# Kernel tuning notes

Measured on AMD Instinct MI355X. Metric: run time of the kernel, lower is better.

Reference implementation:

```python
import jax, jax.numpy as jnp
import numpy as np

N_EMB = 512
DIM = 64
BETA = 0.25
EPS = 1e-10


def setup_inputs() -> dict:
    key = jax.random.key(0)
    k1, k2 = jax.random.split(key)
    z = jax.random.normal(k1, (32, 64, 64, 64), dtype=jnp.float32)  # (B, C=DIM, H, W)
    # embedding weight initialized uniform(-1/K, 1/K) as in the module
    weight = jax.random.uniform(k2, (N_EMB, DIM), dtype=jnp.float32,
                                minval=-1.0 / N_EMB, maxval=1.0 / N_EMB)
    return {"z": z, "weight": weight}


def reference(z, weight):
    # (B,C,H,W) -> (B,H,W,C)
    zp = jnp.transpose(z, (0, 2, 3, 1))
    zf = zp.reshape(-1, DIM)  # (N, D)
    # pairwise squared distances ||z||^2 + ||e||^2 - 2 z.e  -> (N, K)
    d = (jnp.sum(zf * zf, axis=1, keepdims=True)
         + jnp.sum(weight * weight, axis=1)
         - 2.0 * zf @ weight.T)
    codebook = jnp.argmin(d, axis=1)  # (N,)
    encodings = jax.nn.one_hot(codebook, N_EMB, dtype=zf.dtype)  # (N, K)
    # direct gather == one_hot @ weight (same math, efficient form)
    z_q = weight[codebook].reshape(zp.shape)
    sg = jax.lax.stop_gradient
    loss = jnp.mean((sg(z_q) - zp) ** 2) + BETA * jnp.mean((z_q - sg(zp)) ** 2)
    # straight-through estimator
    z_q = zp + sg(z_q - zp)
    e_mean = jnp.mean(encodings, axis=0)
    perplexity = jnp.exp(-jnp.sum(e_mean * jnp.log(e_mean + EPS)))
    z_q = jnp.transpose(z_q, (0, 3, 1, 2))  # back to (B,C,H,W)
    return (loss, z_q, perplexity, encodings, codebook)
```

## Files before the change

### kernel.cpp

```cpp
#include <hip/hip_runtime.h>
#include <math.h>

#define NK 512
#define DIMV 64
#define NPTS (32*64*64)
#define NELEM (32*64*64*64)
#define WT_STRIDE 132

#define OFF_LOSS 0
#define OFF_ZQ   1
#define OFF_PERP (1 + NELEM)
#define OFF_ENC  (2 + NELEM)
#define OFF_CB   (2 + NELEM + (size_t)NPTS * NK)

__global__ __launch_bounds__(256) void vq_main(const float* __restrict__ zg,
                                               const float* __restrict__ wg,
                                               float* __restrict__ out,
                                               int* __restrict__ hist,
                                               double* __restrict__ lossAcc) {
    const int t = threadIdx.x;
    const int blk = blockIdx.x;
    const int b = blk >> 6;
    const int h = blk & 63;

    __shared__ __align__(16) float zt[64 * 64];
    __shared__ __align__(16) float wt[64 * WT_STRIDE];
    __shared__ float aRow[64];
    __shared__ float bnd[128];
    __shared__ int   idxs[64];
    __shared__ float rsum[256];

    float* zqt  = wt;
    float* redv = wt + 4096;
    int*   redi = (int*)(wt + 4096 + 16 * 66);

    {
        const int w = t & 63;
        const int c0 = t >> 6;
        const size_t base = (size_t)b * 262144 + (size_t)h * 64;
        #pragma unroll
        for (int c = c0; c < 64; c += 4)
            zt[c * 64 + w] = zg[base + (size_t)c * 4096 + w];
    }
    __syncthreads();

    if (t < 64) {
        float s = 0.f;
        for (int d = 0; d < 64; ++d) {
            float v = zt[d * 64 + t];
            s = __fadd_rn(s, __fmul_rn(v, v));
        }
        aRow[t] = s;
    }
    __syncthreads();

    const int tx = t & 15;
    const int ty = t >> 4;
    const int ty4 = ty * 4;
    const int tx8 = tx * 8;

    float av[4];
    #pragma unroll
    for (int i = 0; i < 4; ++i) av[i] = aRow[ty4 + i];

    float best[4];
    int bidx[4];
    #pragma unroll
    for (int i = 0; i < 4; ++i) { best[i] = INFINITY; bidx[i] = 0; }

    for (int chunk = 0; chunk < 4; ++chunk) {
        {
            const int d = t & 63, kk0 = t >> 6;
            #pragma unroll
            for (int kk = kk0; kk < 128; kk += 4)
                wt[d * WT_STRIDE + kk] = wg[((size_t)(chunk * 128 + kk)) * 64 + d];
        }
        __syncthreads();

        if (t < 128) {
            float s = 0.f;
            for (int d = 0; d < 64; ++d) {
                float v = wt[d * WT_STRIDE + t];
                s = __fadd_rn(s, __fmul_rn(v, v));
            }
            bnd[t] = s;
        }
        __syncthreads();

        float acc[4][8];
        #pragma unroll
        for (int i = 0; i < 4; ++i)
            #pragma unroll
            for (int j = 0; j < 8; ++j) acc[i][j] = 0.f;

        const float* ztp = zt + ty4;
        const float* wtp = wt + tx8;
        #pragma unroll 4
        for (int d = 0; d < 64; ++d) {
            const float4 zv = *(const float4*)(ztp + d * 64);
            const float4 w0 = *(const float4*)(wtp + d * WT_STRIDE);
            const float4 w1 = *(const float4*)(wtp + d * WT_STRIDE + 4);
            const float zr[4] = {zv.x, zv.y, zv.z, zv.w};
            const float wr[8] = {w0.x, w0.y, w0.z, w0.w, w1.x, w1.y, w1.z, w1.w};
            #pragma unroll
            for (int i = 0; i < 4; ++i)
                #pragma unroll
                for (int j = 0; j < 8; ++j)
                    acc[i][j] = fmaf(zr[i], wr[j], acc[i][j]);
        }

        #pragma unroll
        for (int i = 0; i < 4; ++i) {
            #pragma unroll
            for (int j = 0; j < 8; ++j) {
                float dist = __fsub_rn(__fadd_rn(av[i], bnd[tx8 + j]), 2.0f * acc[i][j]);
                int k = chunk * 128 + tx8 + j;
                if (dist < best[i]) { best[i] = dist; bidx[i] = k; }
            }
        }
        __syncthreads();
    }

    #pragma unroll
    for (int i = 0; i < 4; ++i) {
        redv[tx * 66 + ty4 + i] = best[i];
        redi[tx * 64 + ty4 + i] = bidx[i];
    }
    __syncthreads();

    if (t < 64) {
        float bv = redv[t];
        int bi = redi[t];
        #pragma unroll
        for (int x = 1; x < 16; ++x) {
            float v = redv[x * 66 + t];
            int ii = redi[x * 64 + t];
            if (v < bv || (v == bv && ii < bi)) { bv = v; bi = ii; }
        }
        idxs[t] = bi;
        atomicAdd(&hist[bi], 1);
        out[OFF_CB + (size_t)blk * 64 + t] = (float)bi;
        const float4* wr4 = (const float4*)(wg + (size_t)bi * 64);
        #pragma unroll
        for (int q = 0; q < 16; ++q) {
            float4 v = wr4[q];
            zqt[(4 * q + 0) * 64 + t] = v.x;
            zqt[(4 * q + 1) * 64 + t] = v.y;
            zqt[(4 * q + 2) * 64 + t] = v.z;
            zqt[(4 * q + 3) * 64 + t] = v.w;
        }
    }
    __syncthreads();

    {
        float4* enc = (float4*)(out + OFF_ENC + (size_t)blk * 64 * NK);
        for (int e = t; e < 64 * 128; e += 256) {
            int r = e >> 7, c4 = e & 127;
            int idx = idxs[r];
            float4 v = make_float4(0.f, 0.f, 0.f, 0.f);
            if ((idx >> 2) == c4) ((float*)&v)[idx & 3] = 1.0f;
            enc[(size_t)r * 128 + c4] = v;
        }
    }

    float lsum = 0.f;
    {
        float* zq = out + OFF_ZQ + (size_t)b * 262144 + (size_t)h * 64;
        for (int e = t; e < 4096; e += 256) {
            int p = e & 63, d = e >> 6;
            float zv = zt[d * 64 + p];
            float qv = zqt[d * 64 + p];
            float diff = __fsub_rn(qv, zv);
            lsum = __fadd_rn(lsum, __fmul_rn(diff, diff));
            zq[(size_t)d * 4096 + p] = __fadd_rn(zv, diff);
        }
    }
    rsum[t] = lsum;
    __syncthreads();
    for (int s = 128; s > 0; s >>= 1) {
        if (t < s) rsum[t] += rsum[t + s];
        __syncthreads();
    }
    if (t == 0) atomicAdd(lossAcc, (double)rsum[0]);
}

__global__ __launch_bounds__(512) void vq_finalize(const int* __restrict__ hist,
                                                   const double* __restrict__ lossAcc,
                                                   float* __restrict__ out) {
    __shared__ float sh[512];
    const int t = threadIdx.x;
    float p = (float)hist[t] / (float)NPTS;
    sh[t] = __fmul_rn(p, logf(__fadd_rn(p, 1e-10f)));
    __syncthreads();
    for (int s = 256; s > 0; s >>= 1) {
        if (t < s) sh[t] += sh[t + s];
        __syncthreads();
    }
    if (t == 0) {
        float m = (float)(*lossAcc / (double)NELEM);
        out[OFF_LOSS] = __fadd_rn(m, __fmul_rn(0.25f, m));
        out[OFF_PERP] = expf(-sh[0]);
    }
}

extern "C" void kernel_launch(void* const* d_in, const int* in_sizes, int n_in,
                              void* d_out, int out_size, void* d_ws, size_t ws_size,
                              hipStream_t stream) {
    const float* z = (const float*)d_in[0];
    const float* w = (const float*)d_in[1];
    float* out = (float*)d_out;
    int* hist = (int*)d_ws;
    double* lossAcc = (double*)((char*)d_ws + 2048);

    hipMemsetAsync(d_ws, 0, 4096, stream);
    vq_main<<<2048, 256, 0, stream>>>(z, w, out, hist, lossAcc);
    vq_finalize<<<1, 512, 0, stream>>>(hist, lossAcc, out);
}
```

Before: 472.1 us.

## Precompute transposed codebook and norms, prefetch chunks, vectorize and nontemporal stores

A new prep kernel transposes the codebook into a d-major buffer and computes the codebook norms once, so each main block no longer does strided transposing loads or recomputes norms for every chunk. The main loop prefetches the next codebook chunk into registers while computing the current one, which removes a barrier per chunk. The thread-to-tile mapping is swapped. The encodings and z_q outputs are written with nontemporal vectorized stores, and the loss reduction uses wavefront shuffles instead of a shared-memory tree. The costs are one extra small kernel launch, more registers for the prefetch, and a 128-float LDS stride without padding that may cause bank conflicts.

```diff
diff --git a/kernel.cpp b/kernel.cpp
--- a/kernel.cpp
+++ b/kernel.cpp
@@ -2,10 +2,10 @@
 #include <math.h>
 
 #define NK 512
-#define DIMV 64
 #define NPTS (32*64*64)
 #define NELEM (32*64*64*64)
-#define WT_STRIDE 132
+
+typedef float nvf4 __attribute__((ext_vector_type(4)));
 
 #define OFF_LOSS 0
 #define OFF_ZQ   1
@@ -13,8 +13,41 @@
 #define OFF_ENC  (2 + NELEM)
 #define OFF_CB   (2 + NELEM + (size_t)NPTS * NK)
 
+
+__global__ __launch_bounds__(256) void vq_prep(const float* __restrict__ wg,
+                                               float* __restrict__ wT,
+                                               float* __restrict__ bnd) {
+    __shared__ float tl[64 * 65];
+    const int t = threadIdx.x;
+    const int kbase = blockIdx.x * 64;
+    #pragma unroll
+    for (int it = 0; it < 16; ++it) {
+        int i = it * 256 + t;
+        int k = i >> 6, d = i & 63;
+        tl[k * 65 + d] = wg[(size_t)(kbase + k) * 64 + d];
+    }
+    __syncthreads();
+    #pragma unroll
+    for (int it = 0; it < 16; ++it) {
+        int j = it * 256 + t;
+        int d = j >> 6, kk = j & 63;
+        wT[(size_t)d * 512 + kbase + kk] = tl[kk * 65 + d];
+    }
+    if (t < 64) {
+        float s = 0.f;
+        #pragma unroll 4
+        for (int d = 0; d < 64; ++d) {
+            float v = tl[t * 65 + d];
+            s = __fadd_rn(s, __fmul_rn(v, v));
+        }
+        bnd[kbase + t] = s;
+    }
+}
+
 __global__ __launch_bounds__(256) void vq_main(const float* __restrict__ zg,
                                                const float* __restrict__ wg,
+                                               const float* __restrict__ wT,
+                                               const float* __restrict__ bndg,
                                                float* __restrict__ out,
                                                int* __restrict__ hist,
                                                double* __restrict__ lossAcc) {
@@ -24,15 +57,23 @@
     const int h = blk & 63;
 
     __shared__ __align__(16) float zt[64 * 64];
-    __shared__ __align__(16) float wt[64 * WT_STRIDE];
+    __shared__ __align__(16) float wt[64 * 128];
     __shared__ float aRow[64];
-    __shared__ float bnd[128];
     __shared__ int   idxs[64];
-    __shared__ float rsum[256];
+    __shared__ float wsum[4];
 
     float* zqt  = wt;
     float* redv = wt + 4096;
-    int*   redi = (int*)(wt + 4096 + 16 * 66);
+    int*   redi = (int*)(wt + 4096 + 16 * 68);
+
+    const float4* wT4 = (const float4*)wT;
+    float4* wt4 = (float4*)wt;
+    const int d0 = t >> 5, c4 = t & 31;
+
+    float4 pf[8];
+    #pragma unroll
+    for (int s = 0; s < 8; ++s)
+        pf[s] = wT4[(size_t)(d0 + s * 8) * 128 + c4];
 
     {
         const int w = t & 63;
@@ -56,50 +97,53 @@
 
     const int tx = t & 15;
     const int ty = t >> 4;
-    const int ty4 = ty * 4;
-    const int tx8 = tx * 8;
+    const int p0 = tx * 4;
+    const int ty8 = ty * 8;
 
     float av[4];
     #pragma unroll
-    for (int i = 0; i < 4; ++i) av[i] = aRow[ty4 + i];
+    for (int i = 0; i < 4; ++i) av[i] = aRow[p0 + i];
 
     float best[4];
     int bidx[4];
     #pragma unroll
     for (int i = 0; i < 4; ++i) { best[i] = INFINITY; bidx[i] = 0; }
 
-    for (int chunk = 0; chunk < 4; ++chunk) {
+    for (int c = 0; c < 4; ++c) {
+        if (c) __syncthreads();
+
+        #pragma unroll
+        for (int s = 0; s < 8; ++s)
+            wt4[(d0 + s * 8) * 32 + c4] = pf[s];
+
+        if (c < 3) {
+            #pragma unroll
+            for (int s = 0; s < 8; ++s)
+                pf[s] = wT4[(size_t)(d0 + s * 8) * 128 + (c + 1) * 32 + c4];
+        }
+
+        float bn[8];
         {
-            const int d = t & 63, kk0 = t >> 6;
-            #pragma unroll
-            for (int kk = kk0; kk < 128; kk += 4)
-                wt[d * WT_STRIDE + kk] = wg[((size_t)(chunk * 128 + kk)) * 64 + d];
+            const float4* bp = (const float4*)(bndg + c * 128 + ty8);
+            float4 b0 = bp[0], b1 = bp[1];
+            bn[0] = b0.x; bn[1] = b0.y; bn[2] = b0.z; bn[3] = b0.w;
+            bn[4] = b1.x; bn[5] = b1.y; bn[6] = b1.z; bn[7] = b1.w;
         }
         __syncthreads();
 
-        if (t < 128) {
-            float s = 0.f;
-            for (int d = 0; d < 64; ++d) {
-                float v = wt[d * WT_STRIDE + t];
-                s = __fadd_rn(s, __fmul_rn(v, v));
-            }
-            bnd[t] = s;
-        }
-        __syncthreads();
-
         float acc[4][8];
         #pragma unroll
         for (int i = 0; i < 4; ++i)
             #pragma unroll
             for (int j = 0; j < 8; ++j) acc[i][j] = 0.f;
 
-        const float* ztp = zt + ty4;
-        const float* wtp = wt + tx8;
+        const float* ztp = zt + p0;
+        const float* wtp = wt + ty8;
         #pragma unroll 4
         for (int d = 0; d < 64; ++d) {
             const float4 zv = *(const float4*)(ztp + d * 64);
-            const float4 w0 = *(const float4*)(wtp + d * WT_STRIDE);
-            const float4 w1 = *(const float4*)(wtp + d * WT_STRIDE + 4);
+            const float4 w0 = *(const float4*)(wtp + d * 128);
+            const float4 w1 = *(const float4*)(wtp + d * 128 + 4);
             const float zr[4] = {zv.x, zv.y, zv.z, zv.w};
             const float wr[8] = {w0.x, w0.y, w0.z, w0.w, w1.x, w1.y, w1.z, w1.w};
             #pragma unroll
@@ -113,18 +157,18 @@
         for (int i = 0; i < 4; ++i) {
             #pragma unroll
             for (int j = 0; j < 8; ++j) {
-                float dist = __fsub_rn(__fadd_rn(av[i], bnd[tx8 + j]), 2.0f * acc[i][j]);
-                int k = chunk * 128 + tx8 + j;
+                float dist = __fsub_rn(__fadd_rn(av[i], bn[j]), 2.0f * acc[i][j]);
+                int k = c * 128 + ty8 + j;
                 if (dist < best[i]) { best[i] = dist; bidx[i] = k; }
             }
         }
-        __syncthreads();
-    }
+    }
+    __syncthreads();
 
     #pragma unroll
     for (int i = 0; i < 4; ++i) {
-        redv[tx * 66 + ty4 + i] = best[i];
-        redi[tx * 64 + ty4 + i] = bidx[i];
+        redv[ty * 68 + p0 + i] = best[i];
+        redi[ty * 64 + p0 + i] = bidx[i];
     }
     __syncthreads();
 
@@ -133,7 +177,7 @@
         int bi = redi[t];
         #pragma unroll
         for (int x = 1; x < 16; ++x) {
-            float v = redv[x * 66 + t];
+            float v = redv[x * 68 + t];
             int ii = redi[x * 64 + t];
             if (v < bv || (v == bv && ii < bi)) { bv = v; bi = ii; }
         }
@@ -153,35 +197,44 @@
     __syncthreads();
 
     {
-        float4* enc = (float4*)(out + OFF_ENC + (size_t)blk * 64 * NK);
-        for (int e = t; e < 64 * 128; e += 256) {
-            int r = e >> 7, c4 = e & 127;
+        nvf4* enc = (nvf4*)(out + OFF_ENC + (size_t)blk * 64 * NK);
+        #pragma unroll
+        for (int it = 0; it < 32; ++it) {
+            int e = it * 256 + t;
+            int r = e >> 7, cc = e & 127;
             int idx = idxs[r];
-            float4 v = make_float4(0.f, 0.f, 0.f, 0.f);
-            if ((idx >> 2) == c4) ((float*)&v)[idx & 3] = 1.0f;
-            enc[(size_t)r * 128 + c4] = v;
+            nvf4 v = (nvf4)(0.f);
+            if ((idx >> 2) == cc) v[idx & 3] = 1.0f;
+            __builtin_nontemporal_store(v, &enc[(size_t)r * 128 + cc]);
         }
     }
 
     float lsum = 0.f;
     {
         float* zq = out + OFF_ZQ + (size_t)b * 262144 + (size_t)h * 64;
-        for (int e = t; e < 4096; e += 256) {
-            int p = e & 63, d = e >> 6;
-            float zv = zt[d * 64 + p];
-            float qv = zqt[d * 64 + p];
-            float diff = __fsub_rn(qv, zv);
-            lsum = __fadd_rn(lsum, __fmul_rn(diff, diff));
-            zq[(size_t)d * 4096 + p] = __fadd_rn(zv, diff);
-        }
-    }
-    rsum[t] = lsum;
-    __syncthreads();
-    for (int s = 128; s > 0; s >>= 1) {
-        if (t < s) rsum[t] += rsum[t + s];
-        __syncthreads();
-    }
-    if (t == 0) atomicAdd(lossAcc, (double)rsum[0]);
+        #pragma unroll
+        for (int it = 0; it < 4; ++it) {
+            int f = it * 256 + t;
+            int d = f >> 4, pp = (f & 15) * 4;
+            float4 zv = *(const float4*)(zt + d * 64 + pp);
+            float4 qv = *(const float4*)(zqt + d * 64 + pp);
+            nvf4 o;
+            float dx = __fsub_rn(qv.x, zv.x); lsum = __fadd_rn(lsum, __fmul_rn(dx, dx)); o[0] = __fadd_rn(zv.x, dx);
+            float dy = __fsub_rn(qv.y, zv.y); lsum = __fadd_rn(lsum, __fmul_rn(dy, dy)); o[1] = __fadd_rn(zv.y, dy);
+            float dz = __fsub_rn(qv.z, zv.z); lsum = __fadd_rn(lsum, __fmul_rn(dz, dz)); o[2] = __fadd_rn(zv.z, dz);
+            float dw = __fsub_rn(qv.w, zv.w); lsum = __fadd_rn(lsum, __fmul_rn(dw, dw)); o[3] = __fadd_rn(zv.w, dw);
+            __builtin_nontemporal_store(o, (nvf4*)(zq + (size_t)d * 4096 + pp));
+        }
+    }
+    #pragma unroll
+    for (int off = 32; off > 0; off >>= 1)
+        lsum += __shfl_down(lsum, off);
+    if ((t & 63) == 0) wsum[t >> 6] = lsum;
+    __syncthreads();
+    if (t == 0) {
+        float tot = (wsum[0] + wsum[1]) + (wsum[2] + wsum[3]);
+        atomicAdd(lossAcc, (double)tot);
+    }
 }
 
 __global__ __launch_bounds__(512) void vq_finalize(const int* __restrict__ hist,
@@ -211,8 +264,11 @@
     float* out = (float*)d_out;
     int* hist = (int*)d_ws;
     double* lossAcc = (double*)((char*)d_ws + 2048);
-
-    hipMemsetAsync(d_ws, 0, 4096, stream);
-    vq_main<<<2048, 256, 0, stream>>>(z, w, out, hist, lossAcc);
+    float* wT = (float*)((char*)d_ws + 4096);
+    float* bnd = wT + 64 * 512;
+
+    (void)hipMemsetAsync(d_ws, 0, 4096, stream);
+    vq_prep<<<8, 256, 0, stream>>>(w, wT, bnd);
+    vq_main<<<2048, 256, 0, stream>>>(z, w, wT, bnd, out, hist, lossAcc);
     vq_finalize<<<1, 512, 0, stream>>>(hist, lossAcc, out);
 }
```

New measurement: 467.8 us. About the same (-0.9%).
